# Optimization experiments

Measured on AMD Instinct MI355X. Metric: run time of the kernel, lower is better.

## Reference

```python
import jax, jax.numpy as jnp
import numpy as np

D_MODEL = 16
NHEAD = 4
HEAD_DIM = D_MODEL // NHEAD
DFF = 64
NUM_LAYERS = 2
LN_EPS = 1e-5


def _layer_norm(x, w, b):
    mu = jnp.mean(x, axis=-1, keepdims=True)
    var = jnp.mean(jnp.square(x - mu), axis=-1, keepdims=True)
    return (x - mu) * jax.lax.rsqrt(var + LN_EPS) * w + b


def _encoder_layer(x, Wqkv, bqkv, Wo, bo, ln1w, ln1b, W1, b1, W2, b2, ln2w, ln2b):
    # x: [N, T, D]  (post-norm TransformerEncoderLayer, ReLU, no dropout)
    N, T, D = x.shape
    qkv = x @ Wqkv.T + bqkv                      # [N, T, 3D]
    q, k, v = jnp.split(qkv, 3, axis=-1)
    q = q.reshape(N, T, NHEAD, HEAD_DIM)
    k = k.reshape(N, T, NHEAD, HEAD_DIM)
    v = v.reshape(N, T, NHEAD, HEAD_DIM)
    scale = 1.0 / np.sqrt(HEAD_DIM)
    logits = jnp.einsum('nthd,nshd->nhts', q, k) * scale   # [N, H, T, T]
    attn = jax.nn.softmax(logits, axis=-1)
    ctx = jnp.einsum('nhts,nshd->nthd', attn, v).reshape(N, T, D)
    attn_out = ctx @ Wo.T + bo
    x = _layer_norm(x + attn_out, ln1w, ln1b)
    ff = jax.nn.relu(x @ W1.T + b1) @ W2.T + b2
    x = _layer_norm(x + ff, ln2w, ln2b)
    return x


def setup_inputs() -> dict:
    key = jax.random.key(0)
    ks = jax.random.split(key, 20)
    B, T, H, W = 1, 24, 256, 256
    L = NUM_LAYERS
    s = 0.05
    inp = {
        'x': jax.random.normal(ks[0], (B, T, H, W), dtype=jnp.float32),
        'Win': jax.random.normal(ks[1], (D_MODEL, 1), dtype=jnp.float32) * s,
        'bin': jnp.zeros((D_MODEL,), jnp.float32),
        'Wqkv': jax.random.normal(ks[2], (L, 3 * D_MODEL, D_MODEL), jnp.float32) * s,
        'bqkv': jnp.zeros((L, 3 * D_MODEL), jnp.float32),
        'Wo': jax.random.normal(ks[3], (L, D_MODEL, D_MODEL), jnp.float32) * s,
        'bo': jnp.zeros((L, D_MODEL), jnp.float32),
        'ln1w': jnp.ones((L, D_MODEL), jnp.float32),
        'ln1b': jnp.zeros((L, D_MODEL), jnp.float32),
        'W1': jax.random.normal(ks[4], (L, DFF, D_MODEL), jnp.float32) * s,
        'b1': jnp.zeros((L, DFF), jnp.float32),
        'W2': jax.random.normal(ks[5], (L, D_MODEL, DFF), jnp.float32) * s,
        'b2': jnp.zeros((L, D_MODEL), jnp.float32),
        'ln2w': jnp.ones((L, D_MODEL), jnp.float32),
        'ln2b': jnp.zeros((L, D_MODEL), jnp.float32),
        'Wout': jax.random.normal(ks[6], (1, D_MODEL), jnp.float32) * s,
        'bout': jnp.zeros((1,), jnp.float32),
    }
    return inp


def reference(x, Win, bin, Wqkv, bqkv, Wo, bo, ln1w, ln1b, W1, b1, W2, b2, ln2w, ln2b, Wout, bout):
    B, T, H, W = x.shape
    h = x.transpose(0, 2, 3, 1).reshape(B * H * W, T, 1)
    h = h @ Win.T + bin                              # [N, T, D]
    for l in range(NUM_LAYERS):
        h = _encoder_layer(h, Wqkv[l], bqkv[l], Wo[l], bo[l], ln1w[l], ln1b[l],
                           W1[l], b1[l], W2[l], b2[l], ln2w[l], ln2b[l])
    h = h @ Wout.T + bout                            # [N, T, 1]
    return h.reshape(B, H, W, T).transpose(0, 3, 1, 2)
```

## Files before the change

### kernel.cpp

```cpp
#include <hip/hip_runtime.h>
#include <hip/hip_bf16.h>


#define DM 16
#define NH 4
#define HD 4
#define TT 24
#define DFF 64
#define NSEQ 65536
#define SPB 8
#define BLK 192

typedef __fp16 h2_t  __attribute__((ext_vector_type(2)));
typedef __fp16 f16x4 __attribute__((ext_vector_type(4)));
typedef __fp16 f16x8 __attribute__((ext_vector_type(8)));
typedef float  f32x4 __attribute__((ext_vector_type(4)));

#define MFMA16(A,B,C) __builtin_amdgcn_mfma_f32_16x16x16f16(A,B,C,0,0,0)
#define LGKM0 asm volatile("s_waitcnt lgkmcnt(0)" ::: "memory")

#define OFF_WIN  0
#define OFF_BIN  16
#define OFF_WQKV 32
#define OFF_BQKV 1568
#define OFF_WO   1664
#define OFF_BO   2176
#define OFF_LN1W 2208
#define OFF_LN1B 2240
#define OFF_B1   2272
#define OFF_B2   2400
#define OFF_LN2W 2432
#define OFF_LN2B 2464
#define OFF_WOUT 2496
#define OFF_BOUT 2512
#define OFF_WQH  2516
#define OFF_WOH  3284
#define OFF_W1H  3540
#define OFF_W2H  4564
#define OFF_XBF  5588
#define OFF_DA   5592
#define OFF_WV   5608
#define OFF_W0   5672
#define OFF_WP   5688
#define OFF_C0   5704
#define OFF_SWP  5705
#define OFF_WVO  5706
#define OFF_CVO  5834
#define NDW      5850

#define FOLD 0.7213475204444817f

#define KVH 196
#define TSTR 40
#define XSS 28

__device__ __forceinline__ float fdot2(h2_t a, h2_t b, float c) {
    return __builtin_amdgcn_fdot2(a, b, c, false);
}
__device__ __forceinline__ h2_t pkz(float a, float b) {
    return __builtin_amdgcn_cvt_pkrtz(a, b);
}
__device__ __forceinline__ f16x4 pk4(float a, float b, float c, float d) {
    union { h2_t h[2]; f16x4 v; } u;
    u.h[0] = pkz(a, b); u.h[1] = pkz(c, d);
    return u.v;
}
__device__ __forceinline__ h2_t pkrn(float a, float b) {
    h2_t r; r[0] = (__fp16)a; r[1] = (__fp16)b; return r;
}

__device__ __forceinline__ int x_is_bf16(const unsigned* xw) {
    int ok = 1;
    #pragma unroll
    for (int i = 0; i < 32; ++i) {
        unsigned u = xw[i];
        unsigned e0 = (u >> 7)  & 0xFF;
        unsigned e1 = (u >> 23) & 0xFF;
        ok &= (e0 >= 64u) & (e0 <= 134u) & (e1 >= 64u) & (e1 <= 134u);
    }
    return ok;
}

__global__ __launch_bounds__(256) void cvt_params(
    const void* __restrict__ p0,  const void* __restrict__ p1,
    const void* __restrict__ p2,  const void* __restrict__ p3,
    const void* __restrict__ p4,  const void* __restrict__ p5,
    const void* __restrict__ p6,  const void* __restrict__ p7,
    const void* __restrict__ p8,  const void* __restrict__ p9,
    const void* __restrict__ p10, const void* __restrict__ p11,
    const void* __restrict__ p12, const void* __restrict__ p13,
    const void* __restrict__ p14, const void* __restrict__ p15,
    const void* __restrict__ px,
    float* __restrict__ ws)
{
    const int wbf = (((const unsigned*)p6)[0] == 0x3F803F80u);
    auto ld = [&](const void* p, int j) -> float {
        return wbf ? __bfloat162float(((const __hip_bfloat16*)p)[j])
                   : ((const float*)p)[j];
    };
    unsigned* wsu = (unsigned*)ws;

    if (blockIdx.x == (NDW + 255) / 256) {
        __shared__ float QD[48], QO[48];
        int tid = threadIdx.x;
        if (tid < 48) {
            float acc = 0.f;
            for (int m = 0; m < 16; ++m) acc += ld(p2, tid*16 + m) * ld(p0, m);
            QD[tid] = acc;
        } else if (tid < 96) {
            int j = tid - 48;
            float acc = ld(p3, j);
            for (int m = 0; m < 16; ++m) acc += ld(p2, j*16 + m) * ld(p1, m);
            QO[j] = acc;
        }
        __syncthreads();
        if (tid < 16) {
            int kind = tid >> 2, hh = tid & 3;
            float acc = 0.f;
            for (int j = hh * 4; j < hh * 4 + 4; ++j) {
                float qv = (kind < 2)        ? QD[j]      : QO[j];
                float kv = ((kind & 1) == 0) ? QD[16 + j] : QO[16 + j];
                acc += qv * kv;
            }
            ws[OFF_DA + tid] = acc * FOLD;
        } else if (tid < 80) {
            int k = tid - 16, o = k >> 2, hh = k & 3;
            float acc = 0.f;
            for (int j = hh * 4; j < hh * 4 + 4; ++j)
                acc += ld(p4, o * 16 + j) * QD[32 + j];
            ws[OFF_WV + k] = acc;
        } else if (tid < 96) {
            int o = tid - 80;
            float acc = ld(p5, o);
            for (int j = 0; j < 16; ++j)
                acc += ld(p4, o * 16 + j) * QO[32 + j];
            ws[OFF_W0 + o] = acc;
        }
        if (tid < 128) {
            int o = tid >> 3, dp = tid & 7;
            float a0 = 0.f, a1 = 0.f;
            for (int j = 0; j < 16; ++j) {
                float wo = ld(p4, 256 + o * 16 + j);
                a0 += wo * ld(p2, 768 + (32 + j) * 16 + 2 * dp);
                a1 += wo * ld(p2, 768 + (32 + j) * 16 + 2 * dp + 1);
            }
            union { h2_t h; unsigned u; } cv;
            cv.h = pkrn(a0, a1);
            wsu[OFF_WVO + o * 8 + dp] = cv.u;
        } else if (tid < 144) {
            int o = tid - 128;
            float acc = 0.f;
            for (int j = 0; j < 16; ++j)
                acc += ld(p4, 256 + o * 16 + j) * ld(p3, 80 + j);
            ws[OFF_CVO + o] = acc;
        }
        return;
    }

    int i = blockIdx.x * 256 + threadIdx.x;
    if (i >= NDW) return;
    auto st2 = [&](float a, float b) {
        union { h2_t h; unsigned u; } cv;
        cv.h = pkrn(a, b);
        wsu[i] = cv.u;
    };

    if      (i < OFF_BIN)  { ws[i] = ld(p0, i); }
    else if (i < OFF_WQKV) { ws[i] = ld(p1, i - OFF_BIN); }
    else if (i < OFF_BQKV) {
        int k = i - OFF_WQKV;
        int row = (k >> 4) % 48;
        float v = ld(p2, k);
        if (row < DM) v *= FOLD;
        ws[i] = v;
    }
    else if (i < OFF_WO) {
        int k = i - OFF_BQKV;
        float v = ld(p3, k);
        if (k % 48 < DM) v *= FOLD;
        ws[i] = v;
    }
    else if (i < OFF_BO)   { ws[i] = ld(p4,  i - OFF_WO);   }
    else if (i < OFF_LN1W) { ws[i] = ld(p5,  i - OFF_BO);   }
    else if (i < OFF_LN1B) { ws[i] = ld(p6,  i - OFF_LN1W); }
    else if (i < OFF_B1)   { ws[i] = ld(p7,  i - OFF_LN1B); }
    else if (i < OFF_B2)   { ws[i] = ld(p9,  i - OFF_B1);   }
    else if (i < OFF_LN2W) { ws[i] = ld(p11, i - OFF_B2);   }
    else if (i < OFF_LN2B) { ws[i] = ld(p12, i - OFF_LN2W); }
    else if (i < OFF_WOUT) { ws[i] = ld(p13, i - OFF_LN2B); }
    else if (i < OFF_BOUT) { ws[i] = ld(p14, i - OFF_WOUT); }
    else if (i < OFF_WQH)  { ws[i] = ld(p15, 0); }
    else if (i < OFF_WOH) {
        int k = i - OFF_WQH, l = k / 384, r = (k % 384) / 8, dp = k % 8;
        int j = l * 768 + r * 16 + 2 * dp;
        float s = (r < DM) ? FOLD : 1.f;
        st2(ld(p2, j) * s, ld(p2, j + 1) * s);
    }
    else if (i < OFF_W1H) {
        int k = i - OFF_WOH, l = k / 128, o = (k % 128) / 8, dp = k % 8;
        int j = l * 256 + o * 16 + 2 * dp;
        st2(ld(p4, j), ld(p4, j + 1));
    }
    else if (i < OFF_W2H) {
        int k = i - OFF_W1H, l = k / 512, f = (k % 512) / 8, dp = k % 8;
        int j = l * 1024 + f * 16 + 2 * dp;
        st2(ld(p8, j), ld(p8, j + 1));
    }
    else if (i < OFF_XBF) {
        int k = i - OFF_W2H, l = k / 512, r = k % 512, o = r / 32, fp = r % 32;
        int j = l * 1024 + o * 64 + 2 * fp;
        st2(ld(p10, j), ld(p10, j + 1));
    }
    else if (i < OFF_DA) {
        ws[i] = (i == OFF_XBF) ? (x_is_bf16((const unsigned*)px) ? 1.f : 0.f)
                               : 0.f;
    }
    else if (i < OFF_WP) {  }
    else if (i < OFF_C0) {
        int o = i - OFF_WP;
        ws[i] = ld(p14, o) * ld(p12, 16 + o);
    }
    else if (i == OFF_C0) {
        float acc = ld(p15, 0);
        for (int o = 0; o < 16; ++o) acc += ld(p14, o) * ld(p13, 16 + o);
        ws[i] = acc;
    }
    else if (i == OFF_SWP) {
        float acc = 0.f;
        for (int o = 0; o < 16; ++o) acc += ld(p14, o) * ld(p12, 16 + o);
        ws[i] = acc;
    }
    else {  }
}


__device__ __forceinline__ void ln16(const float* y, const float* w,
                                     const float* b, float* out) {
    float mu = 0.f;
    #pragma unroll
    for (int o = 0; o < DM; ++o) mu += y[o];
    mu *= (1.f / DM);
    float var = 0.f;
    #pragma unroll
    for (int o = 0; o < DM; ++o) { float z = y[o] - mu; var += z * z; }
    float r = rsqrtf(var * (1.f / DM) + 1e-5f);
    #pragma unroll
    for (int o = 0; o < DM; ++o) out[o] = (y[o] - mu) * r * w[o] + b[o];
}

__device__ __forceinline__ void stage_pk(const float* v, __fp16* slab, int lane) {
    #pragma unroll
    for (int m = 0; m < 4; ++m)
        *(f16x4*)(slab + lane * TSTR + m * 8) =
            pk4(v[4*m], v[4*m+1], v[4*m+2], v[4*m+3]);
}

__device__ __forceinline__ void ff_mfma(float* h, int col, int grp, int lane,
        const __fp16* W1h, const __fp16* W2h,
        const float* b1, const float* b2,
        const float* l2w, const float* l2b,
        __fp16* slab)
{
    stage_pk(h, slab, lane);
    LGKM0;
    f16x4 B1[4];
    #pragma unroll
    for (int m = 0; m < 4; ++m)
        B1[m] = *(const f16x4*)(slab + (m*16 + col) * TSTR + grp * 8);
    LGKM0;
    f16x4 A1[4], A2[4];
    f32x4 bb1[4];
    #pragma unroll
    for (int c = 0; c < 4; ++c) {
        A1[c]  = *(const f16x4*)(W1h + (c*16 + col)*16 + grp*4);
        A2[c]  = *(const f16x4*)(W2h + col*64 + c*16 + grp*4);
        bb1[c] = *(const f32x4*)(b1 + c*16 + grp*4);
    }
    const f32x4 b2f = *(const f32x4*)(b2 + grp*4);
    #pragma unroll
    for (int m = 0; m < 4; ++m) {
        f32x4 d1[4];
        #pragma unroll
        for (int c = 0; c < 4; ++c) d1[c] = MFMA16(A1[c], B1[m], bb1[c]);
        f32x4 d2 = b2f;
        #pragma unroll
        for (int c = 0; c < 4; ++c) {
            f16x4 u = pk4(fmaxf(d1[c][0], 0.f), fmaxf(d1[c][1], 0.f),
                          fmaxf(d1[c][2], 0.f), fmaxf(d1[c][3], 0.f));
            d2 = MFMA16(A2[c], u, d2);
        }
        *(f16x4*)(slab + (m*16 + col) * TSTR + grp * 8 + 4) =
            pk4(d2[0], d2[1], d2[2], d2[3]);
    }
    LGKM0;
    float y[DM];
    #pragma unroll
    for (int m = 0; m < 4; ++m) {
        f16x4 a = *(const f16x4*)(slab + lane * TSTR + m * 8 + 4);
        #pragma unroll
        for (int j = 0; j < 4; ++j)
            y[4*m+j] = h[4*m+j] + (float)a[j];
    }
    ln16(y, l2w, l2b, h);
}

__global__ __launch_bounds__(BLK, 3) void tf_kernel(
    const void* __restrict__ xin,
    const float* __restrict__ P,
    void* __restrict__ outp)
{
    __shared__ __align__(16) __fp16 shbuf[7680];
    __shared__ __align__(16) __fp16 qT[BLK * 16];
    __shared__ __align__(16) float xs[SPB * XSS];

    h2_t* Kh = (h2_t*)shbuf;
    h2_t* Vh = Kh + SPB * KVH;

    const __fp16* WqkvH = (const __fp16*)(P + OFF_WQH);
    const __fp16* W1h   = (const __fp16*)(P + OFF_W1H);
    const __fp16* W2h   = (const __fp16*)(P + OFF_W2H);
    const __fp16* Wvoh  = (const __fp16*)(P + OFF_WVO);

    const int tid  = threadIdx.x;
    const int sl   = tid / TT;
    const int t    = tid % TT;
    const int n    = blockIdx.x * SPB + sl;
    const int idx  = t * NSEQ + n;
    const int lane = tid & 63;
    const int wb   = tid & ~63;
    const int col  = lane & 15;
    const int grp  = lane >> 4;

    __fp16* slab = shbuf + (tid >> 6) * (64 * TSTR);

    const int xbf = (P[OFF_XBF] != 0.f);

    float xv;
    if (xbf) xv = __bfloat162float(((const __hip_bfloat16*)xin)[idx]);
    else     xv = ((const float*)xin)[idx];
    xs[sl * XSS + t] = xv;

    float h[DM];
    #pragma unroll
    for (int d = 0; d < DM; ++d)
        h[d] = xv * P[OFF_WIN + d] + P[OFF_BIN + d];
    __syncthreads();

    {
        float f1[NH], f2[NH], sum[NH], sxv[NH];
        #pragma unroll
        for (int hh = 0; hh < NH; ++hh) {
            f1[hh] = P[OFF_DA + hh]     * xv + P[OFF_DA + 8  + hh];
            f2[hh] = P[OFF_DA + 4 + hh] * xv + P[OFF_DA + 12 + hh];
            sum[hh] = 0.f; sxv[hh] = 0.f;
        }
        const f32x4* xp = (const f32x4*)(xs + sl * XSS);
        #pragma unroll
        for (int p = 0; p < 6; ++p) {
            f32x4 x4 = xp[p];
            #pragma unroll
            for (int e = 0; e < 4; ++e) {
                float xvs = x4[e];
                #pragma unroll
                for (int hh = 0; hh < NH; ++hh) {
                    float ee = __builtin_exp2f(f1[hh] * xvs + f2[hh]);
                    sum[hh] += ee;
                    sxv[hh] += ee * xvs;
                }
            }
        }
        float m1[NH];
        #pragma unroll
        for (int hh = 0; hh < NH; ++hh)
            m1[hh] = sxv[hh] * __builtin_amdgcn_rcpf(sum[hh]);

        float y[DM];
        #pragma unroll
        for (int o = 0; o < DM; ++o) {
            f32x4 wv = *(const f32x4*)(P + OFF_WV + o * 4);
            y[o] = h[o] + P[OFF_W0 + o]
                 + m1[0]*wv[0] + m1[1]*wv[1] + m1[2]*wv[2] + m1[3]*wv[3];
        }
        ln16(y, P + OFF_LN1W, P + OFF_LN1B, h);

        ff_mfma(h, col, grp, lane, W1h, W2h,
                P + OFF_B1, P + OFF_B2, P + OFF_LN2W, P + OFF_LN2B, slab);
    }

    {
        const __fp16* WqH1 = WqkvH + 768;
        const float*  bq   = P + OFF_BQKV + 48;

        stage_pk(h, slab, lane);
        LGKM0;
        f16x4 B[4];
        #pragma unroll
        for (int m = 0; m < 4; ++m)
            B[m] = *(const f16x4*)(slab + (m*16 + col) * TSTR + grp * 8);
        f16x4 Aq  = *(const f16x4*)(WqH1 + col * DM + grp * 4);
        f16x4 Ak  = *(const f16x4*)(WqH1 + (16 + col) * DM + grp * 4);
        f16x4 Avo = *(const f16x4*)(Wvoh + col * DM + grp * 4);
        f32x4 Cq  = *(const f32x4*)(bq + grp * 4);
        f32x4 Ck  = *(const f32x4*)(bq + 16 + grp * 4);
        f32x4 Cvo = *(const f32x4*)(P + OFF_CVO + grp * 4);
        f32x4 dq[4], dk[4], dv[4];
        #pragma unroll
        for (int m = 0; m < 4; ++m) {
            dq[m] = MFMA16(Aq,  B[m], Cq);
            dk[m] = MFMA16(Ak,  B[m], Ck);
            dv[m] = MFMA16(Avo, B[m], Cvo);
        }
        __syncthreads();
        #pragma unroll
        for (int m = 0; m < 4; ++m) {
            int bt = wb + m * 16 + col;
            int s2 = bt / TT, t2 = bt - s2 * TT;
            union { h2_t h[2]; unsigned u[2]; } kk;
            kk.h[0] = pkz(dk[m][0], dk[m][1]);
            kk.h[1] = pkz(dk[m][2], dk[m][3]);
            *(h2_t*)(Kh + s2 * KVH + grp * 48 + 2 * t2)     = kk.h[0];
            *(h2_t*)(Kh + s2 * KVH + grp * 48 + 2 * t2 + 1) = kk.h[1];
            __fp16* Vhh = (__fp16*)(Vh + s2 * KVH + grp * 48);
            #pragma unroll
            for (int j = 0; j < 4; ++j)
                Vhh[j * 24 + t2] = (__fp16)dv[m][j];
            *(f16x4*)(qT + bt * 16 + grp * 4) =
                pk4(dq[m][0], dq[m][1], dq[m][2], dq[m][3]);
        }
        __syncthreads();

        h2_t q2[8];
        {
            union { f16x8 v; h2_t h[4]; } qlo, qhi;
            qlo.v = *(const f16x8*)(qT + tid * 16);
            qhi.v = *(const f16x8*)(qT + tid * 16 + 8);
            #pragma unroll
            for (int m = 0; m < 4; ++m) { q2[m] = qlo.h[m]; q2[4+m] = qhi.h[m]; }
        }

        float ctx[DM];
        h2_t one2; one2[0] = (__fp16)1.f; one2[1] = (__fp16)1.f;
        #pragma unroll
        for (int hh = 0; hh < NH; ++hh) {
            const h2_t qa = q2[2*hh], qb = q2[2*hh+1];
            const h2_t* Kp = Kh + sl * KVH + hh * 48;
            h2_t e2[12];
            float sum = 0.f;
            #pragma unroll
            for (int p = 0; p < 12; ++p) {
                union { f16x8 v; h2_t h[4]; } kk;
                kk.v = *(const f16x8*)(Kp + 4*p);
                float d0 = fdot2(qb, kk.h[1], fdot2(qa, kk.h[0], 0.f));
                float d1 = fdot2(qb, kk.h[3], fdot2(qa, kk.h[2], 0.f));
                e2[p] = pkz(__builtin_exp2f(d0), __builtin_exp2f(d1));
                sum = fdot2(e2[p], one2, sum);
            }
            float inv = __builtin_amdgcn_rcpf(sum);
            const h2_t* Vp = Vh + sl * KVH + hh * 48;
            #pragma unroll
            for (int o = 0; o < 4; ++o) {
                union { f16x8 v; h2_t h[4]; } v0, v1;
                v0.v = *(const f16x8*)(Vp + o*12);
                v1.v = *(const f16x8*)(Vp + o*12 + 4);
                union { f16x4 v; h2_t h[2]; } v2;
                v2.v = *(const f16x4*)(Vp + o*12 + 8);
                float c = 0.f;
                #pragma unroll
                for (int p = 0; p < 4; ++p) c = fdot2(e2[p],     v0.h[p], c);
                #pragma unroll
                for (int p = 0; p < 4; ++p) c = fdot2(e2[4 + p], v1.h[p], c);
                c = fdot2(e2[8], v2.h[0], c);
                c = fdot2(e2[9], v2.h[1], c);
                union { f16x4 v; h2_t h[2]; } v3;
                v3.v = *(const f16x4*)(Vp + o*12 + 10);
                c = fdot2(e2[10], v3.h[0], c);
                c = fdot2(e2[11], v3.h[1], c);
                ctx[hh*4 + o] = c * inv;
            }
        }
        __syncthreads();

        {
            const float* bo1 = P + OFF_BO + 16;
            float y[DM];
            #pragma unroll
            for (int o = 0; o < DM; ++o)
                y[o] = h[o] + ctx[o] + bo1[o];
            ln16(y, P + OFF_LN1W + 16, P + OFF_LN1B + 16, h);
        }

        {
            stage_pk(h, slab, lane);
            LGKM0;
            f16x4 B1[4];
            #pragma unroll
            for (int m = 0; m < 4; ++m)
                B1[m] = *(const f16x4*)(slab + (m*16 + col) * TSTR + grp * 8);
            LGKM0;
            const __fp16* W1f = W1h + 1024;
            const __fp16* W2f = W2h + 1024;
            const float*  b1  = P + OFF_B1 + 64;
            f16x4 A1[4], A2[4];
            f32x4 bb1[4];
            #pragma unroll
            for (int c = 0; c < 4; ++c) {
                A1[c]  = *(const f16x4*)(W1f + (c*16 + col)*16 + grp*4);
                A2[c]  = *(const f16x4*)(W2f + col*64 + c*16 + grp*4);
                bb1[c] = *(const f32x4*)(b1 + c*16 + grp*4);
            }
            const f32x4 b2f = *(const f32x4*)(P + OFF_B2 + 16 + grp*4);
            #pragma unroll
            for (int m = 0; m < 4; ++m) {
                f32x4 d1[4];
                #pragma unroll
                for (int c = 0; c < 4; ++c) d1[c] = MFMA16(A1[c], B1[m], bb1[c]);
                f32x4 d2 = b2f;
                #pragma unroll
                for (int c = 0; c < 4; ++c) {
                    f16x4 u = pk4(fmaxf(d1[c][0], 0.f), fmaxf(d1[c][1], 0.f),
                                  fmaxf(d1[c][2], 0.f), fmaxf(d1[c][3], 0.f));
                    d2 = MFMA16(A2[c], u, d2);
                }
                *(f16x4*)(slab + (m*16 + col) * TSTR + grp * 8 + 4) =
                    pk4(d2[0], d2[1], d2[2], d2[3]);
            }
            LGKM0;
            float y[DM];
            #pragma unroll
            for (int m = 0; m < 4; ++m) {
                f16x4 a = *(const f16x4*)(slab + lane * TSTR + m * 8 + 4);
                #pragma unroll
                for (int j = 0; j < 4; ++j) y[4*m+j] = h[4*m+j] + (float)a[j];
            }
            float mu = 0.f;
            #pragma unroll
            for (int o = 0; o < DM; ++o) mu += y[o];
            mu *= (1.f / DM);
            float var = 0.f;
            #pragma unroll
            for (int o = 0; o < DM; ++o) { float z = y[o] - mu; var += z * z; }
            float r = rsqrtf(var * (1.f / DM) + 1e-5f);
            float dotv = 0.f;
            #pragma unroll
            for (int o = 0; o < DM; ++o) dotv += P[OFF_WP + o] * y[o];
            float outv = P[OFF_C0] + r * (dotv - mu * P[OFF_SWP]);
            if (xbf) ((__hip_bfloat16*)outp)[idx] = __float2bfloat16(outv);
            else     ((float*)outp)[idx] = outv;
        }
    }
}

extern "C" void kernel_launch(void* const* d_in, const int* in_sizes, int n_in,
                              void* d_out, int out_size, void* d_ws, size_t ws_size,
                              hipStream_t stream) {
    float* P = (float*)d_ws;

    cvt_params<<<(NDW + 255) / 256 + 1, 256, 0, stream>>>(
        d_in[1],  d_in[2],  d_in[3],  d_in[4],
        d_in[5],  d_in[6],  d_in[7],  d_in[8],
        d_in[9],  d_in[10], d_in[11], d_in[12],
        d_in[13], d_in[14], d_in[15], d_in[16],
        d_in[0],
        P);

    tf_kernel<<<NSEQ / SPB, BLK, 0, stream>>>(d_in[0], P, d_out);
}
```

Baseline: 230.5 us.

## Stage input/output through shared memory, drop softmax shift term, pad qT

Global input loads and output stores now go through the shared xs buffer, so each thread touches contiguous sequence elements. In the bf16 path a thread moves two values per 32-bit access. The per-query constant f2 is removed from the exp2 in the first layer's attention, which relies on softmax being unchanged by a constant shift across keys. The qT shared buffer gets a padded stride to reduce LDS bank conflicts. The cost is an extra barrier and shared-memory round trip at both the start and the end of the kernel.

```diff
diff --git a/kernel.cpp b/kernel.cpp
--- a/kernel.cpp
+++ b/kernel.cpp
@@ -52,6 +52,7 @@
 
 #define KVH 196
 #define TSTR 40
+#define QTS 20
 #define XSS 28
 
 __device__ __forceinline__ float fdot2(h2_t a, h2_t b, float c) {
@@ -310,7 +311,7 @@
     void* __restrict__ outp)
 {
     __shared__ __align__(16) __fp16 shbuf[7680];
-    __shared__ __align__(16) __fp16 qT[BLK * 16];
+    __shared__ __align__(16) __fp16 qT[BLK * QTS];
     __shared__ __align__(16) float xs[SPB * XSS];
 
     h2_t* Kh = (h2_t*)shbuf;
@@ -324,8 +325,7 @@
     const int tid  = threadIdx.x;
     const int sl   = tid / TT;
     const int t    = tid % TT;
-    const int n    = blockIdx.x * SPB + sl;
-    const int idx  = t * NSEQ + n;
+    const int n0   = blockIdx.x * SPB;
     const int lane = tid & 63;
     const int wb   = tid & ~63;
     const int col  = lane & 15;
@@ -335,23 +335,35 @@
 
     const int xbf = (P[OFF_XBF] != 0.f);
 
-    float xv;
-    if (xbf) xv = __bfloat162float(((const __hip_bfloat16*)xin)[idx]);
-    else     xv = ((const float*)xin)[idx];
-    xs[sl * XSS + t] = xv;
-
+    if (xbf) {
+        if (tid < 96) {
+            int tt = tid >> 2, qd = tid & 3;
+            unsigned u = *(const unsigned*)((const char*)xin +
+                (size_t)tt * NSEQ * 2 + (size_t)n0 * 2 + qd * 4);
+            union { unsigned u; float f; } lo, hi;
+            lo.u = (u & 0xFFFFu) << 16;
+            hi.u = u & 0xFFFF0000u;
+            xs[(2*qd)     * XSS + tt] = lo.f;
+            xs[(2*qd + 1) * XSS + tt] = hi.f;
+        }
+    } else {
+        int tt = tid >> 3, s = tid & 7;
+        xs[s * XSS + tt] =
+            ((const float*)xin)[(size_t)tt * NSEQ + n0 + s];
+    }
+    __syncthreads();
+
+    const float xv = xs[sl * XSS + t];
     float h[DM];
     #pragma unroll
     for (int d = 0; d < DM; ++d)
         h[d] = xv * P[OFF_WIN + d] + P[OFF_BIN + d];
-    __syncthreads();
 
     {
-        float f1[NH], f2[NH], sum[NH], sxv[NH];
+        float f1[NH], sum[NH], sxv[NH];
         #pragma unroll
         for (int hh = 0; hh < NH; ++hh) {
-            f1[hh] = P[OFF_DA + hh]     * xv + P[OFF_DA + 8  + hh];
-            f2[hh] = P[OFF_DA + 4 + hh] * xv + P[OFF_DA + 12 + hh];
+            f1[hh] = P[OFF_DA + hh] * xv + P[OFF_DA + 8 + hh];
             sum[hh] = 0.f; sxv[hh] = 0.f;
         }
         const f32x4* xp = (const f32x4*)(xs + sl * XSS);
@@ -363,7 +375,7 @@
                 float xvs = x4[e];
                 #pragma unroll
                 for (int hh = 0; hh < NH; ++hh) {
-                    float ee = __builtin_exp2f(f1[hh] * xvs + f2[hh]);
+                    float ee = __builtin_exp2f(f1[hh] * xvs);
                     sum[hh] += ee;
                     sxv[hh] += ee * xvs;
                 }
@@ -387,6 +399,7 @@
                 P + OFF_B1, P + OFF_B2, P + OFF_LN2W, P + OFF_LN2B, slab);
     }
 
+    float outv;
     {
         const __fp16* WqH1 = WqkvH + 768;
         const float*  bq   = P + OFF_BQKV + 48;
@@ -424,7 +437,7 @@
             #pragma unroll
             for (int j = 0; j < 4; ++j)
                 Vhh[j * 24 + t2] = (__fp16)dv[m][j];
-            *(f16x4*)(qT + bt * 16 + grp * 4) =
+            *(f16x4*)(qT + bt * QTS + grp * 4) =
                 pk4(dq[m][0], dq[m][1], dq[m][2], dq[m][3]);
         }
         __syncthreads();
@@ -432,8 +445,8 @@
         h2_t q2[8];
         {
             union { f16x8 v; h2_t h[4]; } qlo, qhi;
-            qlo.v = *(const f16x8*)(qT + tid * 16);
-            qhi.v = *(const f16x8*)(qT + tid * 16 + 8);
+            qlo.v = *(const f16x8*)(qT + tid * QTS);
+            qhi.v = *(const f16x8*)(qT + tid * QTS + 8);
             #pragma unroll
             for (int m = 0; m < 4; ++m) { q2[m] = qlo.h[m]; q2[4+m] = qhi.h[m]; }
         }
@@ -543,10 +556,25 @@
             float dotv = 0.f;
             #pragma unroll
             for (int o = 0; o < DM; ++o) dotv += P[OFF_WP + o] * y[o];
-            float outv = P[OFF_C0] + r * (dotv - mu * P[OFF_SWP]);
-            if (xbf) ((__hip_bfloat16*)outp)[idx] = __float2bfloat16(outv);
-            else     ((float*)outp)[idx] = outv;
-        }
+            outv = P[OFF_C0] + r * (dotv - mu * P[OFF_SWP]);
+        }
+    }
+
+    xs[sl * XSS + t] = outv;
+    __syncthreads();
+    if (xbf) {
+        if (tid < 96) {
+            int tt = tid >> 2, qd = tid & 3;
+            __hip_bfloat16 b0 = __float2bfloat16(xs[(2*qd)     * XSS + tt]);
+            __hip_bfloat16 b1 = __float2bfloat16(xs[(2*qd + 1) * XSS + tt]);
+            unsigned u = (unsigned)(*(unsigned short*)&b0)
+                       | ((unsigned)(*(unsigned short*)&b1) << 16);
+            *(unsigned*)((char*)outp +
+                (size_t)tt * NSEQ * 2 + (size_t)n0 * 2 + qd * 4) = u;
+        }
+    } else {
+        int tt = tid >> 3, s = tid & 7;
+        ((float*)outp)[(size_t)tt * NSEQ + n0 + s] = xs[s * XSS + tt];
     }
 }
 
```

Result: no change. 231.6 us (+0.5%).
